# Performance work log

Measured on AMD Instinct MI355X. Metric: run time of the kernel, lower is better.

The kernel has to match this reference:

```python
import jax, jax.numpy as jnp
import numpy as np
import math

H = 1024      # hidden_size
NH = 32       # nhead
DH = H // NH  # head dim (== NH by construction, required for broadcasting)
SF = 0.2      # scaling_factor
B, S = 1, 48  # batch, seq_len (Sq == Sk required)


def setup_inputs() -> dict:
    key = jax.random.key(0)
    ks = jax.random.split(key, 9)
    sd = 1.0 / math.sqrt(H)
    return {
        "q": jax.random.normal(ks[0], (B, S, H), jnp.float32),
        "k": jax.random.normal(ks[1], (B, S, H), jnp.float32),
        "v": jax.random.normal(ks[2], (B, S, H), jnp.float32),
        "Wq": jax.random.normal(ks[3], (H, H), jnp.float32) * sd,
        "bq": jax.random.normal(ks[4], (H,), jnp.float32) * sd,
        "Wk": jax.random.normal(ks[5], (H, H), jnp.float32) * sd,
        "bk": jax.random.normal(ks[6], (H,), jnp.float32) * sd,
        "Wv": jax.random.normal(ks[7], (H, H), jnp.float32) * sd,
        "bv": jax.random.normal(ks[8], (H,), jnp.float32) * sd,
        "dropout_p": 0,
    }


def reference(q, k, v, Wq, bq, Wk, bk, Wv, bv, dropout_p):
    inv_sqrt_h = 1.0 / math.sqrt(H)
    qp = q @ Wq.T + bq  # [B,S,H]
    kp = k @ Wk.T + bk
    vp = v @ Wv.T + bv

    def heads(x):
        # view(-1, S, NH, DH).transpose(0,1) -> [S, B, NH, DH]
        return jnp.swapaxes(x.reshape(-1, x.shape[1], NH, DH), 0, 1)

    qh = heads(qp) * inv_sqrt_h          # [S,B,NH,DH]
    kh = heads(kp)
    vh = heads(vp)

    _sq = jnp.sum(qh * qh, axis=-1)      # [S,B,NH]
    # k^T @ q over the head axis: [S,B,DH,NH] @ [S,B,NH,DH] -> [S,B,DH,DH]
    _sk = jnp.matmul(jnp.swapaxes(kh, -1, -2), qh) * inv_sqrt_h

    # broadcast: [S,B,NH,1] + [S,B,DH,DH,1] + |[S,B,DH,DH]-[S,B,NH,1]|*SF
    # with B=1, DH==NH -> _s: [S,S,NH,NH,NH]
    _s = (_sq[..., None] + _sk[..., None]
          + jnp.abs(jnp.swapaxes(_sk, -1, -2) - _sq[..., None]) * SF)
    attn = jax.nn.softmax(_s, axis=-1)   # [S,S,NH,NH,NH]
    # dropout_p == 0 -> identity (matches `if dropout_p > 0` in torch source)

    out = jnp.matmul(attn, vh)           # batch-broadcast matmul -> [S,S,NH,NH,NH]
    out = jnp.swapaxes(out, 0, 1)
    return out.reshape(out.shape[1], -1)  # [S, S*NH^3]
```

## Files before the change

### kernel.cpp

```cpp
#include <hip/hip_runtime.h>

constexpr int kH  = 1024;
constexpr int kS  = 48;
constexpr int kNH = 32;
constexpr int kDH = 32;
constexpr float kSF = 0.2f;
constexpr int kRepsPerRow = kS * kNH;
constexpr int kRowF4      = kRepsPerRow * 256;

constexpr int kKC = 8;
constexpr size_t kPartialFloats = (size_t)kKC * 3 * kS * kH;

typedef float f32x4 __attribute__((ext_vector_type(4)));

__device__ __forceinline__ f32x4 ld4v(const float* p) {
    return *reinterpret_cast<const f32x4*>(p);
}
__device__ __forceinline__ float dot4v(f32x4 a, f32x4 b) {
    return a.x * b.x + a.y * b.y + a.z * b.z + a.w * b.w;
}
__device__ __forceinline__ float4 ld4(const float* p) {
    return *reinterpret_cast<const float4*>(p);
}
__device__ __forceinline__ float dot4(float4 a, float4 b) {
    return a.x * b.x + a.y * b.y + a.z * b.z + a.w * b.w;
}

__global__ __launch_bounds__(512) void proj_split_kernel(
    const float* __restrict__ q, const float* __restrict__ k, const float* __restrict__ v,
    const float* __restrict__ Wq, const float* __restrict__ Wk, const float* __restrict__ Wv,
    float* __restrict__ partial)
{
    const int bid = blockIdx.x;
    const int g   = bid >> 6;
    const int rem = bid & 63;
    const int ot  = rem >> 3;
    const int kc  = rem & 7;
    const int o0  = ot * 128;
    const int k0  = kc * 128;
    const float* X = (g == 0) ? q : (g == 1) ? k : v;
    const float* W = (g == 0) ? Wq : (g == 1) ? Wk : Wv;

    __shared__ float Xs[kS][128];
    const int t = threadIdx.x;

#pragma unroll
    for (int r = 0; r < 3; ++r) {
        const int slot = r * 512 + t;
        const int s  = slot >> 5;
        const int kq = slot & 31;
        *reinterpret_cast<f32x4*>(&Xs[s][kq * 4]) = ld4v(X + s * kH + k0 + kq * 4);
    }
    __syncthreads();

    const int og    = t & 31;
    const int sbase = (t >> 5) * 3;

    float acc[3][4] = {};
    const float* w0p = W + (o0 + og      ) * kH + k0;
    const float* w1p = W + (o0 + og + 32 ) * kH + k0;
    const float* w2p = W + (o0 + og + 64 ) * kH + k0;
    const float* w3p = W + (o0 + og + 96 ) * kH + k0;

#pragma unroll 4
    for (int kq = 0; kq < 32; ++kq) {
        const f32x4 w0 = ld4v(w0p + kq * 4);
        const f32x4 w1 = ld4v(w1p + kq * 4);
        const f32x4 w2 = ld4v(w2p + kq * 4);
        const f32x4 w3 = ld4v(w3p + kq * 4);
#pragma unroll
        for (int i = 0; i < 3; ++i) {
            const f32x4 xv = *reinterpret_cast<const f32x4*>(&Xs[sbase + i][kq * 4]);
            acc[i][0] += dot4v(xv, w0);
            acc[i][1] += dot4v(xv, w1);
            acc[i][2] += dot4v(xv, w2);
            acc[i][3] += dot4v(xv, w3);
        }
    }

    float* P = partial + (size_t)(kc * 3 + g) * kS * kH;
#pragma unroll
    for (int i = 0; i < 3; ++i)
#pragma unroll
        for (int j = 0; j < 4; ++j)
            P[(sbase + i) * kH + o0 + og + j * 32] = acc[i][j];
}

__global__ __launch_bounds__(256) void proj_kernel(
    const float* __restrict__ q, const float* __restrict__ k, const float* __restrict__ v,
    const float* __restrict__ Wq, const float* __restrict__ bq,
    const float* __restrict__ Wk, const float* __restrict__ bk,
    const float* __restrict__ Wv, const float* __restrict__ bv,
    float* __restrict__ ws)
{
    const int wid  = blockIdx.x * 4 + (threadIdx.x >> 6);
    const int lane = threadIdx.x & 63;
    const int g = wid >> 10;
    const int o = wid & 1023;

    const float *X, *W, *Bv;
    if (g == 0)      { X = q; W = Wq; Bv = bq; }
    else if (g == 1) { X = k; W = Wk; Bv = bk; }
    else             { X = v; W = Wv; Bv = bv; }
    float* OUT = ws + g * (kS * kH);

    const float* wr = W + o * kH + lane * 4;
    const float4 w0 = ld4(wr);
    const float4 w1 = ld4(wr + 256);
    const float4 w2 = ld4(wr + 512);
    const float4 w3 = ld4(wr + 768);

    float acc[kS];
#pragma unroll
    for (int s = 0; s < kS; ++s) {
        const float* xr = X + s * kH + lane * 4;
        acc[s] = dot4(ld4(xr), w0) + dot4(ld4(xr + 256), w1)
               + dot4(ld4(xr + 512), w2) + dot4(ld4(xr + 768), w3);
    }
#pragma unroll
    for (int s = 0; s < kS; ++s) {
        float a = acc[s];
        a += __shfl_xor(a, 1);
        a += __shfl_xor(a, 2);
        a += __shfl_xor(a, 4);
        a += __shfl_xor(a, 8);
        a += __shfl_xor(a, 16);
        a += __shfl_xor(a, 32);
        acc[s] = a;
    }
    if (lane == 0) {
        const float bo = Bv[o];
#pragma unroll
        for (int s = 0; s < kS; ++s) OUT[s * kH + o] = acc[s] + bo;
    }
}

template <bool SPLIT>
__global__ __launch_bounds__(256) void fused_kernel(
    const float* __restrict__ src,
    const float* __restrict__ bq, const float* __restrict__ bk,
    const float* __restrict__ bv,
    float* __restrict__ out)
{
    const int x  = blockIdx.x / 96;
    const int rb = blockIdx.x % 96;
    const int t  = threadIdx.x;

    __shared__ float qrow[kH];
    __shared__ float krow[kH];
    __shared__ float vrow[kH];
    __shared__ float sq[kNH];
    __shared__ float sk[kDH][kDH];
    __shared__ float pT[kNH][kNH];

    if constexpr (SPLIT) {
        f32x4 aq = ld4v(bq + t * 4);
        f32x4 ak = ld4v(bk + t * 4);
        f32x4 av = ld4v(bv + t * 4);
#pragma unroll
        for (int kc = 0; kc < kKC; ++kc) {
            const float* base = src + (size_t)(kc * 3) * kS * kH + (size_t)x * kH + t * 4;
            aq += ld4v(base);
            ak += ld4v(base + (size_t)kS * kH);
            av += ld4v(base + (size_t)2 * kS * kH);
        }
        *reinterpret_cast<f32x4*>(&qrow[t * 4]) = aq;
        *reinterpret_cast<f32x4*>(&krow[t * 4]) = ak;
        *reinterpret_cast<f32x4*>(&vrow[t * 4]) = av;
    } else {
        reinterpret_cast<float4*>(qrow)[t] = ld4(src + x * kH + t * 4);
        reinterpret_cast<float4*>(krow)[t] = ld4(src + (kS + x) * kH + t * 4);
        reinterpret_cast<float4*>(vrow)[t] = ld4(src + (2 * kS + x) * kH + t * 4);
    }
    __syncthreads();

    if (t < kNH) {
        float a = 0.f;
#pragma unroll
        for (int d = 0; d < kDH; ++d) {
            float xq = qrow[t * kDH + d];
            a += xq * xq;
        }
        sq[t] = a * (1.0f / 1024.0f);
    }
    {
        const int d = t >> 3;
        const int eq = t & 7;
        float4 a = {0.f, 0.f, 0.f, 0.f};
#pragma unroll
        for (int n = 0; n < kNH; ++n) {
            const float kv = krow[n * kDH + d];
            const float4 qv = reinterpret_cast<const float4*>(qrow)[n * 8 + eq];
            a.x += kv * qv.x; a.y += kv * qv.y; a.z += kv * qv.z; a.w += kv * qv.w;
        }
        const float sc = 1.0f / 1024.0f;
        a.x *= sc; a.y *= sc; a.z *= sc; a.w *= sc;
        *reinterpret_cast<float4*>(&sk[d][eq * 4]) = a;
    }
    __syncthreads();

    {
        const int b = t >> 3;
        const int c0 = (t & 7) * 4;
        const float s0 = sq[b];
        float v0 = kSF * fabsf(sk[c0 + 0][b] - s0);
        float v1 = kSF * fabsf(sk[c0 + 1][b] - s0);
        float v2 = kSF * fabsf(sk[c0 + 2][b] - s0);
        float v3 = kSF * fabsf(sk[c0 + 3][b] - s0);
        float m = fmaxf(fmaxf(v0, v1), fmaxf(v2, v3));
        m = fmaxf(m, __shfl_xor(m, 1));
        m = fmaxf(m, __shfl_xor(m, 2));
        m = fmaxf(m, __shfl_xor(m, 4));
        float e0 = __expf(v0 - m);
        float e1 = __expf(v1 - m);
        float e2 = __expf(v2 - m);
        float e3 = __expf(v3 - m);
        float sum = e0 + e1 + e2 + e3;
        sum += __shfl_xor(sum, 1);
        sum += __shfl_xor(sum, 2);
        sum += __shfl_xor(sum, 4);
        const float inv = 1.0f / sum;
        pT[c0 + 0][b] = e0 * inv;
        pT[c0 + 1][b] = e1 * inv;
        pT[c0 + 2][b] = e2 * inv;
        pT[c0 + 3][b] = e3 * inv;
    }
    __syncthreads();

    {
        const int b = t >> 3;
        const int dq = t & 7;
        float4 acc = {0.f, 0.f, 0.f, 0.f};
#pragma unroll
        for (int c = 0; c < kNH; ++c) {
            const float pv = pT[c][b];
            const float4 vv = reinterpret_cast<const float4*>(vrow)[c * 8 + dq];
            acc.x += pv * vv.x; acc.y += pv * vv.y; acc.z += pv * vv.z; acc.w += pv * vv.w;
        }
        reinterpret_cast<float4*>(qrow)[t] = acc;
    }
    __syncthreads();

    {
        const int w = t >> 6;
        const int l = t & 63;
        const f32x4* OshF4 = reinterpret_cast<const f32x4*>(qrow);
        const f32x4 o0 = OshF4[0 * 64 + l];
        const f32x4 o1 = OshF4[1 * 64 + l];
        const f32x4 o2 = OshF4[2 * 64 + l];
        const f32x4 o3 = OshF4[3 * 64 + l];

        f32x4* base = reinterpret_cast<f32x4*>(out)
                    + (size_t)x * kRowF4 + (size_t)(rb * 16 + w * 4) * 256 + l;
#pragma unroll
        for (int rep = 0; rep < 4; ++rep) {
            f32x4* p = base + rep * 256;
            __builtin_nontemporal_store(o0, p);
            __builtin_nontemporal_store(o1, p + 64);
            __builtin_nontemporal_store(o2, p + 128);
            __builtin_nontemporal_store(o3, p + 192);
        }
    }
}

extern "C" void kernel_launch(void* const* d_in, const int* in_sizes, int n_in,
                              void* d_out, int out_size, void* d_ws, size_t ws_size,
                              hipStream_t stream)
{
    (void)in_sizes; (void)n_in; (void)out_size;
    const float* q  = (const float*)d_in[0];
    const float* k  = (const float*)d_in[1];
    const float* v  = (const float*)d_in[2];
    const float* Wq = (const float*)d_in[3];
    const float* bq = (const float*)d_in[4];
    const float* Wk = (const float*)d_in[5];
    const float* bk = (const float*)d_in[6];
    const float* Wv = (const float*)d_in[7];
    const float* bv = (const float*)d_in[8];

    float* ws  = (float*)d_ws;
    float* out = (float*)d_out;

    if (ws_size >= kPartialFloats * sizeof(float)) {
        proj_split_kernel<<<192, 512, 0, stream>>>(q, k, v, Wq, Wk, Wv, ws);
        fused_kernel<true><<<kS * 96, 256, 0, stream>>>(ws, bq, bk, bv, out);
    } else {
        proj_kernel<<<768, 256, 0, stream>>>(q, k, v, Wq, bq, Wk, bk, Wv, bv, ws);
        fused_kernel<false><<<kS * 96, 256, 0, stream>>>(ws, bq, bk, bv, out);
    }
}
```

Measured before the change: 96.39 us.

## Compute attention once per row and broadcast in a separate kernel

```diff
diff --git a/kernel.cpp b/kernel.cpp
--- a/kernel.cpp
+++ b/kernel.cpp
@@ -10,6 +10,7 @@
 
 constexpr int kKC = 8;
 constexpr size_t kPartialFloats = (size_t)kKC * 3 * kS * kH;
+constexpr size_t kNeedFloats    = kPartialFloats + (size_t)kS * kH;
 
 typedef float f32x4 __attribute__((ext_vector_type(4)));
 
@@ -86,65 +87,14 @@
             P[(sbase + i) * kH + o0 + og + j * 32] = acc[i][j];
 }
 
-__global__ __launch_bounds__(256) void proj_kernel(
-    const float* __restrict__ q, const float* __restrict__ k, const float* __restrict__ v,
-    const float* __restrict__ Wq, const float* __restrict__ bq,
-    const float* __restrict__ Wk, const float* __restrict__ bk,
-    const float* __restrict__ Wv, const float* __restrict__ bv,
-    float* __restrict__ ws)
-{
-    const int wid  = blockIdx.x * 4 + (threadIdx.x >> 6);
-    const int lane = threadIdx.x & 63;
-    const int g = wid >> 10;
-    const int o = wid & 1023;
-
-    const float *X, *W, *Bv;
-    if (g == 0)      { X = q; W = Wq; Bv = bq; }
-    else if (g == 1) { X = k; W = Wk; Bv = bk; }
-    else             { X = v; W = Wv; Bv = bv; }
-    float* OUT = ws + g * (kS * kH);
-
-    const float* wr = W + o * kH + lane * 4;
-    const float4 w0 = ld4(wr);
-    const float4 w1 = ld4(wr + 256);
-    const float4 w2 = ld4(wr + 512);
-    const float4 w3 = ld4(wr + 768);
-
-    float acc[kS];
-#pragma unroll
-    for (int s = 0; s < kS; ++s) {
-        const float* xr = X + s * kH + lane * 4;
-        acc[s] = dot4(ld4(xr), w0) + dot4(ld4(xr + 256), w1)
-               + dot4(ld4(xr + 512), w2) + dot4(ld4(xr + 768), w3);
-    }
-#pragma unroll
-    for (int s = 0; s < kS; ++s) {
-        float a = acc[s];
-        a += __shfl_xor(a, 1);
-        a += __shfl_xor(a, 2);
-        a += __shfl_xor(a, 4);
-        a += __shfl_xor(a, 8);
-        a += __shfl_xor(a, 16);
-        a += __shfl_xor(a, 32);
-        acc[s] = a;
-    }
-    if (lane == 0) {
-        const float bo = Bv[o];
-#pragma unroll
-        for (int s = 0; s < kS; ++s) OUT[s * kH + o] = acc[s] + bo;
-    }
-}
-
-template <bool SPLIT>
-__global__ __launch_bounds__(256) void fused_kernel(
-    const float* __restrict__ src,
+__global__ __launch_bounds__(256) void reduce_attn_kernel(
+    const float* __restrict__ partial,
     const float* __restrict__ bq, const float* __restrict__ bk,
     const float* __restrict__ bv,
-    float* __restrict__ out)
-{
-    const int x  = blockIdx.x / 96;
-    const int rb = blockIdx.x % 96;
-    const int t  = threadIdx.x;
+    float* __restrict__ O)
+{
+    const int x = blockIdx.x;
+    const int t = threadIdx.x;
 
     __shared__ float qrow[kH];
     __shared__ float krow[kH];
@@ -153,13 +103,13 @@
     __shared__ float sk[kDH][kDH];
     __shared__ float pT[kNH][kNH];
 
-    if constexpr (SPLIT) {
+    {
         f32x4 aq = ld4v(bq + t * 4);
         f32x4 ak = ld4v(bk + t * 4);
         f32x4 av = ld4v(bv + t * 4);
 #pragma unroll
         for (int kc = 0; kc < kKC; ++kc) {
-            const float* base = src + (size_t)(kc * 3) * kS * kH + (size_t)x * kH + t * 4;
+            const float* base = partial + (size_t)(kc * 3) * kS * kH + (size_t)x * kH + t * 4;
             aq += ld4v(base);
             ak += ld4v(base + (size_t)kS * kH);
             av += ld4v(base + (size_t)2 * kS * kH);
@@ -167,10 +117,6 @@
         *reinterpret_cast<f32x4*>(&qrow[t * 4]) = aq;
         *reinterpret_cast<f32x4*>(&krow[t * 4]) = ak;
         *reinterpret_cast<f32x4*>(&vrow[t * 4]) = av;
-    } else {
-        reinterpret_cast<float4*>(qrow)[t] = ld4(src + x * kH + t * 4);
-        reinterpret_cast<float4*>(krow)[t] = ld4(src + (kS + x) * kH + t * 4);
-        reinterpret_cast<float4*>(vrow)[t] = ld4(src + (2 * kS + x) * kH + t * 4);
     }
     __syncthreads();
 
@@ -237,10 +183,165 @@
             const float4 vv = reinterpret_cast<const float4*>(vrow)[c * 8 + dq];
             acc.x += pv * vv.x; acc.y += pv * vv.y; acc.z += pv * vv.z; acc.w += pv * vv.w;
         }
+        reinterpret_cast<float4*>(O + x * kH)[t] = acc;
+    }
+}
+
+__global__ __launch_bounds__(256) void bcast_kernel(
+    const float* __restrict__ O, float* __restrict__ out)
+{
+    const int x  = blockIdx.x / 96;
+    const int rb = blockIdx.x % 96;
+    const int w  = threadIdx.x >> 6;
+    const int l  = threadIdx.x & 63;
+
+    const f32x4* Orow = reinterpret_cast<const f32x4*>(O + x * kH);
+    const f32x4 o0 = Orow[0 * 64 + l];
+    const f32x4 o1 = Orow[1 * 64 + l];
+    const f32x4 o2 = Orow[2 * 64 + l];
+    const f32x4 o3 = Orow[3 * 64 + l];
+
+    f32x4* base = reinterpret_cast<f32x4*>(out)
+                + (size_t)x * kRowF4 + (size_t)(rb * 16 + w * 4) * 256 + l;
+#pragma unroll
+    for (int rep = 0; rep < 4; ++rep) {
+        f32x4* p = base + rep * 256;
+        __builtin_nontemporal_store(o0, p);
+        __builtin_nontemporal_store(o1, p + 64);
+        __builtin_nontemporal_store(o2, p + 128);
+        __builtin_nontemporal_store(o3, p + 192);
+    }
+}
+
+__global__ __launch_bounds__(256) void proj_kernel(
+    const float* __restrict__ q, const float* __restrict__ k, const float* __restrict__ v,
+    const float* __restrict__ Wq, const float* __restrict__ bq,
+    const float* __restrict__ Wk, const float* __restrict__ bk,
+    const float* __restrict__ Wv, const float* __restrict__ bv,
+    float* __restrict__ ws)
+{
+    const int wid  = blockIdx.x * 4 + (threadIdx.x >> 6);
+    const int lane = threadIdx.x & 63;
+    const int g = wid >> 10;
+    const int o = wid & 1023;
+
+    const float *X, *W, *Bv;
+    if (g == 0)      { X = q; W = Wq; Bv = bq; }
+    else if (g == 1) { X = k; W = Wk; Bv = bk; }
+    else             { X = v; W = Wv; Bv = bv; }
+    float* OUT = ws + g * (kS * kH);
+
+    const float* wr = W + o * kH + lane * 4;
+    const float4 w0 = ld4(wr);
+    const float4 w1 = ld4(wr + 256);
+    const float4 w2 = ld4(wr + 512);
+    const float4 w3 = ld4(wr + 768);
+
+    float acc[kS];
+#pragma unroll
+    for (int s = 0; s < kS; ++s) {
+        const float* xr = X + s * kH + lane * 4;
+        acc[s] = dot4(ld4(xr), w0) + dot4(ld4(xr + 256), w1)
+               + dot4(ld4(xr + 512), w2) + dot4(ld4(xr + 768), w3);
+    }
+#pragma unroll
+    for (int s = 0; s < kS; ++s) {
+        float a = acc[s];
+        a += __shfl_xor(a, 1);
+        a += __shfl_xor(a, 2);
+        a += __shfl_xor(a, 4);
+        a += __shfl_xor(a, 8);
+        a += __shfl_xor(a, 16);
+        a += __shfl_xor(a, 32);
+        acc[s] = a;
+    }
+    if (lane == 0) {
+        const float bo = Bv[o];
+#pragma unroll
+        for (int s = 0; s < kS; ++s) OUT[s * kH + o] = acc[s] + bo;
+    }
+}
+
+__global__ __launch_bounds__(256) void fused_fallback_kernel(
+    const float* __restrict__ ws, float* __restrict__ out)
+{
+    const int x  = blockIdx.x / 96;
+    const int rb = blockIdx.x % 96;
+    const int t  = threadIdx.x;
+
+    __shared__ float qrow[kH];
+    __shared__ float krow[kH];
+    __shared__ float vrow[kH];
+    __shared__ float sq[kNH];
+    __shared__ float sk[kDH][kDH];
+    __shared__ float pT[kNH][kNH];
+
+    reinterpret_cast<float4*>(qrow)[t] = ld4(ws + x * kH + t * 4);
+    reinterpret_cast<float4*>(krow)[t] = ld4(ws + (kS + x) * kH + t * 4);
+    reinterpret_cast<float4*>(vrow)[t] = ld4(ws + (2 * kS + x) * kH + t * 4);
+    __syncthreads();
+
+    if (t < kNH) {
+        float a = 0.f;
+#pragma unroll
+        for (int d = 0; d < kDH; ++d) { float xq = qrow[t * kDH + d]; a += xq * xq; }
+        sq[t] = a * (1.0f / 1024.0f);
+    }
+    {
+        const int d = t >> 3;
+        const int eq = t & 7;
+        float4 a = {0.f, 0.f, 0.f, 0.f};
+#pragma unroll
+        for (int n = 0; n < kNH; ++n) {
+            const float kv = krow[n * kDH + d];
+            const float4 qv = reinterpret_cast<const float4*>(qrow)[n * 8 + eq];
+            a.x += kv * qv.x; a.y += kv * qv.y; a.z += kv * qv.z; a.w += kv * qv.w;
+        }
+        const float sc = 1.0f / 1024.0f;
+        a.x *= sc; a.y *= sc; a.z *= sc; a.w *= sc;
+        *reinterpret_cast<float4*>(&sk[d][eq * 4]) = a;
+    }
+    __syncthreads();
+    {
+        const int b = t >> 3;
+        const int c0 = (t & 7) * 4;
+        const float s0 = sq[b];
+        float v0 = kSF * fabsf(sk[c0 + 0][b] - s0);
+        float v1 = kSF * fabsf(sk[c0 + 1][b] - s0);
+        float v2 = kSF * fabsf(sk[c0 + 2][b] - s0);
+        float v3 = kSF * fabsf(sk[c0 + 3][b] - s0);
+        float m = fmaxf(fmaxf(v0, v1), fmaxf(v2, v3));
+        m = fmaxf(m, __shfl_xor(m, 1));
+        m = fmaxf(m, __shfl_xor(m, 2));
+        m = fmaxf(m, __shfl_xor(m, 4));
+        float e0 = __expf(v0 - m);
+        float e1 = __expf(v1 - m);
+        float e2 = __expf(v2 - m);
+        float e3 = __expf(v3 - m);
+        float sum = e0 + e1 + e2 + e3;
+        sum += __shfl_xor(sum, 1);
+        sum += __shfl_xor(sum, 2);
+        sum += __shfl_xor(sum, 4);
+        const float inv = 1.0f / sum;
+        pT[c0 + 0][b] = e0 * inv;
+        pT[c0 + 1][b] = e1 * inv;
+        pT[c0 + 2][b] = e2 * inv;
+        pT[c0 + 3][b] = e3 * inv;
+    }
+    __syncthreads();
+    {
+        const int b = t >> 3;
+        const int dq = t & 7;
+        float4 acc = {0.f, 0.f, 0.f, 0.f};
+#pragma unroll
+        for (int c = 0; c < kNH; ++c) {
+            const float pv = pT[c][b];
+            const float4 vv = reinterpret_cast<const float4*>(vrow)[c * 8 + dq];
+            acc.x += pv * vv.x; acc.y += pv * vv.y; acc.z += pv * vv.z; acc.w += pv * vv.w;
+        }
         reinterpret_cast<float4*>(qrow)[t] = acc;
     }
     __syncthreads();
-
     {
         const int w = t >> 6;
         const int l = t & 63;
@@ -249,7 +350,6 @@
         const f32x4 o1 = OshF4[1 * 64 + l];
         const f32x4 o2 = OshF4[2 * 64 + l];
         const f32x4 o3 = OshF4[3 * 64 + l];
-
         f32x4* base = reinterpret_cast<f32x4*>(out)
                     + (size_t)x * kRowF4 + (size_t)(rb * 16 + w * 4) * 256 + l;
 #pragma unroll
@@ -281,11 +381,13 @@
     float* ws  = (float*)d_ws;
     float* out = (float*)d_out;
 
-    if (ws_size >= kPartialFloats * sizeof(float)) {
+    if (ws_size >= kNeedFloats * sizeof(float)) {
+        float* O = ws + kPartialFloats;
         proj_split_kernel<<<192, 512, 0, stream>>>(q, k, v, Wq, Wk, Wv, ws);
-        fused_kernel<true><<<kS * 96, 256, 0, stream>>>(ws, bq, bk, bv, out);
+        reduce_attn_kernel<<<kS, 256, 0, stream>>>(ws, bq, bk, bv, O);
+        bcast_kernel<<<kS * 96, 256, 0, stream>>>(O, out);
     } else {
         proj_kernel<<<768, 256, 0, stream>>>(q, k, v, Wq, bq, Wk, bk, Wv, bv, ws);
-        fused_kernel<false><<<kS * 96, 256, 0, stream>>>(ws, bq, bk, bv, out);
-    }
-}
+        fused_fallback_kernel<<<kS * 96, 256, 0, stream>>>(ws, out);
+    }
+}
```

Result: slower. 100.1 us (+3.9%).
